# Kernel tuning notes

Measured on AMD Instinct MI355X. Metric: run time of the kernel, lower is better.

The kernel has to match this reference:

```python
import jax, jax.numpy as jnp
import numpy as np

T, B, H, L = 512, 32, 512, 2  # seq_len, batch, hidden_size, num_layers (input_size == H)


def _lstm_layer(x, Wih, Whh, bih, bhh):
    """x: [T,B,D]; Wih: [4H,D]; Whh: [4H,H]; biases: [4H]. Returns [T,B,H]."""
    # Precompute input contribution for all timesteps (one big GEMM).
    x_proj = jnp.einsum('tbd,gd->tbg', x, Wih) + bih + bhh  # [T,B,4H]
    h0 = jnp.zeros((x.shape[1], H), x.dtype)
    c0 = jnp.zeros((x.shape[1], H), x.dtype)

    def step(carry, xp):
        h, c = carry
        z = xp + h @ Whh.T  # [B,4H]
        i = jax.nn.sigmoid(z[:, 0 * H:1 * H])
        f = jax.nn.sigmoid(z[:, 1 * H:2 * H])
        g = jnp.tanh(z[:, 2 * H:3 * H])
        o = jax.nn.sigmoid(z[:, 3 * H:4 * H])
        c_new = f * c + i * g
        h_new = o * jnp.tanh(c_new)
        return (h_new, c_new), h_new

    (_, _), ys = jax.lax.scan(step, (h0, c0), x_proj)
    return ys  # [T,B,H]


def setup_inputs() -> dict:
    key = jax.random.key(0)
    k1, k2, k3, k4, k5 = jax.random.split(key, 5)
    scale = 1.0 / np.sqrt(H)  # torch Linear default init range ~ U(-1/sqrt(fan_in), ...)
    return {
        'seq_inputs': jax.random.normal(k1, (T, B, H), jnp.float32),
        'W_ih': jax.random.normal(k2, (L, 4 * H, H), jnp.float32) * scale,
        'W_hh': jax.random.normal(k3, (L, 4 * H, H), jnp.float32) * scale,
        'b_ih': jax.random.normal(k4, (L, 4 * H), jnp.float32) * scale,
        'b_hh': jax.random.normal(k5, (L, 4 * H), jnp.float32) * scale,
    }


def reference(seq_inputs, W_ih, W_hh, b_ih, b_hh):
    x = seq_inputs
    for l in range(L):  # small fixed layer loop
        x = _lstm_layer(x, W_ih[l], W_hh[l], b_ih[l], b_hh[l])
    return x  # [T,B,H] last-layer hidden sequence
```

## Files before the change

### kernel.cpp

```cpp
#include <hip/hip_runtime.h>


typedef _Float16 half8_t __attribute__((ext_vector_type(8)));
typedef _Float16 half4_t __attribute__((ext_vector_type(4)));
typedef float f32x4 __attribute__((ext_vector_type(4)));
typedef unsigned int u32;
typedef unsigned short u16;

#define T_LEN 512
#define BATCH 32
#define HID 512
#define SLOT 16384
#define LW (2048 * 512)

__device__ __forceinline__ float fast_sigmoid(float x) {
  return 1.f / (1.f + __expf(-x));
}
__device__ __forceinline__ float fast_tanh(float x) {
  return 1.f - 2.f / (1.f + __expf(2.f * x));
}
__device__ __forceinline__ u32 epoch_peek(const u32* p) {
  return __hip_atomic_load(p, __ATOMIC_RELAXED, __HIP_MEMORY_SCOPE_AGENT);
}

__global__ __launch_bounds__(256) void convert_k(
    const float4* __restrict__ x,
    const float4* __restrict__ wih,
    const float4* __restrict__ whh,
    const float* __restrict__ bih, const float* __restrict__ bhh,
    half4_t* __restrict__ xh, half4_t* __restrict__ wihh, half4_t* __restrict__ whhh,
    float* __restrict__ bsum) {
  const int N4X = 2097152, N4W = 524288, TOT = N4X + 2 * N4W;
  int gid = blockIdx.x * 256 + threadIdx.x;
  for (int i = gid; i < TOT; i += gridDim.x * 256) {
    float4 v;
    half4_t* dst;
    if (i < N4X) { v = x[i]; dst = xh + i; }
    else if (i < N4X + N4W) { v = wih[i - N4X]; dst = wihh + (i - N4X); }
    else { v = whh[i - N4X - N4W]; dst = whhh + (i - N4X - N4W); }
    half4_t h;
    h[0] = (_Float16)v.x; h[1] = (_Float16)v.y; h[2] = (_Float16)v.z; h[3] = (_Float16)v.w;
    *dst = h;
  }
  if (gid < 4096) bsum[gid] = bih[gid] + bhh[gid];
}

__global__ __launch_bounds__(128, 1) void lstm_fused(
    const _Float16* __restrict__ x0h,
    const _Float16* __restrict__ wih16,
    const _Float16* __restrict__ whh16,
    const float* __restrict__ bsum,
    _Float16* h0seq,
    _Float16* h1seq,
    u32* epoch0, u32* epoch1,
    float* outf) {
  int bid = blockIdx.x;
  int layer = bid >> 6, wg = bid & 63;
  int tid = threadIdx.x;
  int ln = tid & 63;
  int q = ln >> 4, l15 = ln & 15;
  int m0 = (tid >> 6) * 16;

  const _Float16* wih_l = wih16 + (size_t)layer * LW;
  const _Float16* whh_l = whh16 + (size_t)layer * LW;
  half8_t wx[2][16], wh[2][16];
  float bv[2];
#pragma unroll
  for (int j = 0; j < 2; ++j) {
    int nl = j * 16 + l15;
    int grow = (nl >> 3) * 512 + wg * 8 + (nl & 7);
    size_t ro = (size_t)grow * 512;
#pragma unroll
    for (int kc = 0; kc < 16; ++kc) {
      wx[j][kc] = *(const half8_t*)(wih_l + ro + kc * 32 + q * 8);
      wh[j][kc] = *(const half8_t*)(whh_l + ro + kc * 32 + q * 8);
    }
    bv[j] = bsum[layer * 2048 + grow];
  }

  const _Float16* xbase = layer ? (h0seq + SLOT) : x0h;
  _Float16* hself = layer ? h1seq : h0seq;
  u32* eself = layer ? epoch1 : epoch0;

  int cb = tid >> 2;
  int cp = tid & 3;
  int col0 = wg * 8 + cp * 2;
  float cst0 = 0.f, cst1 = 0.f;

  __shared__ float Zs[4 * 297];

  for (int t = 1; t <= T_LEN; ++t) {
    const _Float16* xsrc = xbase + (size_t)(t - 1) * SLOT;
    const _Float16* hsrc = hself + (size_t)(t - 1) * SLOT;
    f32x4 acc0 = {}, acc1 = {};
    half8_t af[16];

    if (layer == 0) {
#pragma unroll
      for (int kc = 0; kc < 16; ++kc)
        af[kc] = *(const half8_t*)(xsrc + (m0 + l15) * HID + kc * 32 + q * 8);
#pragma unroll
      for (int kc = 0; kc < 16; ++kc) {
        acc0 = __builtin_amdgcn_mfma_f32_16x16x32_f16(af[kc], wx[0][kc], acc0, 0, 0, 0);
        acc1 = __builtin_amdgcn_mfma_f32_16x16x32_f16(af[kc], wx[1][kc], acc1, 0, 0, 0);
      }
      u32 tgt = 64u * (u32)(t - 1);
      while (epoch_peek(epoch0) < tgt) { __builtin_amdgcn_s_sleep(1); }
      asm volatile("" ::: "memory");
    } else {
      u32 tgt0 = 64u * (u32)t, tgt1 = 64u * (u32)(t - 1);
      while (epoch_peek(epoch0) < tgt0 || epoch_peek(epoch1) < tgt1) {
        __builtin_amdgcn_s_sleep(1);
      }
      asm volatile("" ::: "memory");
#pragma unroll
      for (int kc = 0; kc < 16; ++kc)
        af[kc] = *(const half8_t*)(xsrc + (m0 + l15) * HID + kc * 32 + q * 8);
#pragma unroll
      for (int kc = 0; kc < 16; ++kc) {
        acc0 = __builtin_amdgcn_mfma_f32_16x16x32_f16(af[kc], wx[0][kc], acc0, 0, 0, 0);
        acc1 = __builtin_amdgcn_mfma_f32_16x16x32_f16(af[kc], wx[1][kc], acc1, 0, 0, 0);
      }
    }

#pragma unroll
    for (int kc = 0; kc < 16; ++kc)
      af[kc] = *(const half8_t*)(hsrc + (m0 + l15) * HID + kc * 32 + q * 8);
#pragma unroll
    for (int kc = 0; kc < 16; ++kc) {
      acc0 = __builtin_amdgcn_mfma_f32_16x16x32_f16(af[kc], wh[0][kc], acc0, 0, 0, 0);
      acc1 = __builtin_amdgcn_mfma_f32_16x16x32_f16(af[kc], wh[1][kc], acc1, 0, 0, 0);
    }

#pragma unroll
    for (int j = 0; j < 2; ++j) {
      int nl = j * 16 + l15, g = nl >> 3, c = nl & 7;
      const f32x4& a = j ? acc1 : acc0;
#pragma unroll
      for (int r = 0; r < 4; ++r)
        Zs[g * 297 + (m0 + q * 4 + r) * 9 + c] = a[r] + bv[j];
    }
    __syncthreads();

    float h0, h1;
    {
      float zi0 = Zs[0 * 297 + cb * 9 + cp * 2], zi1 = Zs[0 * 297 + cb * 9 + cp * 2 + 1];
      float zf0 = Zs[1 * 297 + cb * 9 + cp * 2], zf1 = Zs[1 * 297 + cb * 9 + cp * 2 + 1];
      float zg0 = Zs[2 * 297 + cb * 9 + cp * 2], zg1 = Zs[2 * 297 + cb * 9 + cp * 2 + 1];
      float zo0 = Zs[3 * 297 + cb * 9 + cp * 2], zo1 = Zs[3 * 297 + cb * 9 + cp * 2 + 1];
      float i0 = fast_sigmoid(zi0), f0 = fast_sigmoid(zf0), g0 = fast_tanh(zg0), o0 = fast_sigmoid(zo0);
      float i1 = fast_sigmoid(zi1), f1 = fast_sigmoid(zf1), g1 = fast_tanh(zg1), o1 = fast_sigmoid(zo1);
      cst0 = f0 * cst0 + i0 * g0;
      cst1 = f1 * cst1 + i1 * g1;
      h0 = o0 * fast_tanh(cst0);
      h1 = o1 * fast_tanh(cst1);
      u32 hp = (u32)__builtin_bit_cast(u16, (_Float16)h0) |
               ((u32)__builtin_bit_cast(u16, (_Float16)h1) << 16);
      u32* hdst = (u32*)(hself + (size_t)t * SLOT + cb * HID + col0);
      __hip_atomic_store(hdst, hp, __ATOMIC_RELAXED, __HIP_MEMORY_SCOPE_AGENT);
    }
    __syncthreads();
    if (tid == 0)
      (void)__hip_atomic_fetch_add(eself, 1u, __ATOMIC_RELAXED, __HIP_MEMORY_SCOPE_AGENT);
    if (layer) {
      float2 o2; o2.x = h0; o2.y = h1;
      *(float2*)(outf + (size_t)(t - 1) * SLOT + cb * HID + col0) = o2;
    }
  }
}

extern "C" void kernel_launch(void* const* d_in, const int* in_sizes, int n_in,
                              void* d_out, int out_size, void* d_ws, size_t ws_size,
                              hipStream_t stream) {
  const float* x = (const float*)d_in[0];
  const float* Wih = (const float*)d_in[1];
  const float* Whh = (const float*)d_in[2];
  const float* bih = (const float*)d_in[3];
  const float* bhh = (const float*)d_in[4];
  char* ws = (char*)d_ws;
  const size_t OFF_X0H = 0;
  const size_t OFF_H0SEQ = 16777216;
  const size_t OFF_H1SEQ = 33587200;
  const size_t OFF_WIH = 50397184;
  const size_t OFF_WHH = 54591488;
  const size_t OFF_BSUM = 58785792;
  const size_t OFF_EPOCH0 = 58802176;
  const size_t OFF_EPOCH1 = 58802432;
  const size_t TOTAL = 58802688;
  if (ws_size < TOTAL) return;
  _Float16* x0h = (_Float16*)(ws + OFF_X0H);
  _Float16* h0seq = (_Float16*)(ws + OFF_H0SEQ);
  _Float16* h1seq = (_Float16*)(ws + OFF_H1SEQ);
  _Float16* wihh = (_Float16*)(ws + OFF_WIH);
  _Float16* whhh = (_Float16*)(ws + OFF_WHH);
  float* bsum = (float*)(ws + OFF_BSUM);
  u32* epoch0 = (u32*)(ws + OFF_EPOCH0);
  u32* epoch1 = (u32*)(ws + OFF_EPOCH1);

  hipMemsetAsync(ws + OFF_EPOCH0, 0, 512, stream);
  hipMemsetAsync(ws + OFF_H0SEQ, 0, 32768, stream);
  hipMemsetAsync(ws + OFF_H1SEQ, 0, 32768, stream);
  convert_k<<<3072, 256, 0, stream>>>((const float4*)x, (const float4*)Wih,
                                      (const float4*)Whh, bih, bhh,
                                      (half4_t*)x0h, (half4_t*)wihh, (half4_t*)whhh, bsum);
  lstm_fused<<<128, 128, 0, stream>>>(x0h, wihh, whhh, bsum, h0seq, h1seq,
                                      epoch0, epoch1, (float*)d_out);
}
```

Before: 3.388 ms.

## Precompute layer-0 input projection with a tiled GEMM and relax per-step barriers

Layer 0's input contribution is now computed for all timesteps up front by a separate LDS-tiled MFMA GEMM (fp16 output with biases folded in), so the recurrent loop only does the Whh matmul for layer 0. Layer 0 prefetches its projected gates before spinning on the epoch counter. The Zs scratch is double-buffered by step parity, which lets the trailing __syncthreads be replaced by a vmcnt wait plus a per-wave epoch increment, with targets doubled to 128. The cost is an extra kernel, a 64MB fp16 intermediate, and fp16 rounding of the preactivations.

```diff
diff --git a/kernel.cpp b/kernel.cpp
--- a/kernel.cpp
+++ b/kernel.cpp
@@ -3,6 +3,7 @@
 
 typedef _Float16 half8_t __attribute__((ext_vector_type(8)));
 typedef _Float16 half4_t __attribute__((ext_vector_type(4)));
+typedef _Float16 half2_t __attribute__((ext_vector_type(2)));
 typedef float f32x4 __attribute__((ext_vector_type(4)));
 typedef unsigned int u32;
 typedef unsigned short u16;
@@ -22,80 +23,163 @@
 __device__ __forceinline__ u32 epoch_peek(const u32* p) {
   return __hip_atomic_load(p, __ATOMIC_RELAXED, __HIP_MEMORY_SCOPE_AGENT);
 }
-
-__global__ __launch_bounds__(256) void convert_k(
-    const float4* __restrict__ x,
-    const float4* __restrict__ wih,
-    const float4* __restrict__ whh,
-    const float* __restrict__ bih, const float* __restrict__ bhh,
-    half4_t* __restrict__ xh, half4_t* __restrict__ wihh, half4_t* __restrict__ whhh,
-    float* __restrict__ bsum) {
-  const int N4X = 2097152, N4W = 524288, TOT = N4X + 2 * N4W;
+__device__ __forceinline__ void async_copy16(const void* gsrc, void* ldst) {
+  __builtin_amdgcn_global_load_lds(
+      (const __attribute__((address_space(1))) u32*)gsrc,
+      (__attribute__((address_space(3))) u32*)ldst,
+      16, 0, 0);
+}
+
+__global__ __launch_bounds__(256) void convert_w(
+    const float4* __restrict__ wih, const float4* __restrict__ whh,
+    half4_t* __restrict__ wihh, half4_t* __restrict__ whhh) {
+  const int N4W = 524288;
   int gid = blockIdx.x * 256 + threadIdx.x;
-  for (int i = gid; i < TOT; i += gridDim.x * 256) {
+  for (int i = gid; i < 2 * N4W; i += gridDim.x * 256) {
     float4 v;
     half4_t* dst;
-    if (i < N4X) { v = x[i]; dst = xh + i; }
-    else if (i < N4X + N4W) { v = wih[i - N4X]; dst = wihh + (i - N4X); }
-    else { v = whh[i - N4X - N4W]; dst = whhh + (i - N4X - N4W); }
+    if (i < N4W) { v = wih[i]; dst = wihh + i; }
+    else { v = whh[i - N4W]; dst = whhh + (i - N4W); }
     half4_t h;
     h[0] = (_Float16)v.x; h[1] = (_Float16)v.y; h[2] = (_Float16)v.z; h[3] = (_Float16)v.w;
     *dst = h;
   }
-  if (gid < 4096) bsum[gid] = bih[gid] + bhh[gid];
+}
+
+__global__ __launch_bounds__(256) void gemm_xproj(
+    const float* __restrict__ A, const _Float16* __restrict__ W,
+    const float* __restrict__ bih, const float* __restrict__ bhh,
+    _Float16* __restrict__ C) {
+  __shared__ _Float16 As[128 * 64];
+  __shared__ _Float16 Bs[128 * 64];
+  int bx = blockIdx.x;
+  int tn = bx & 15, tm = bx >> 4;
+  int m0 = tm * 128, n0 = tn * 128;
+  int tid = threadIdx.x, wv = tid >> 6, ln = tid & 63;
+  int wm = wv & 1, wn = wv >> 1;
+  int q = ln >> 4, cc = ln & 15;
+  int am = tid >> 1, afq0 = (tid & 1) * 8;
+  f32x4 acc[4][4] = {};
+  for (int k0 = 0; k0 < 512; k0 += 64) {
+#pragma unroll
+    for (int i = 0; i < 8; ++i) {
+      int fq = afq0 + i;
+      float4 v = *(const float4*)(A + (size_t)(m0 + am) * 512 + k0 + fq * 4);
+      half4_t h;
+      h[0] = (_Float16)v.x; h[1] = (_Float16)v.y; h[2] = (_Float16)v.z; h[3] = (_Float16)v.w;
+      int c = fq >> 1, sub = fq & 1;
+      *(half4_t*)(As + am * 64 + (c ^ (am & 7)) * 8 + sub * 4) = h;
+    }
+#pragma unroll
+    for (int j = 0; j < 4; ++j) {
+      int p = (wv * 4 + j) * 64 + ln;
+      int m = p >> 3, pc = p & 7, kg = pc ^ (m & 7);
+      async_copy16(W + (size_t)(n0 + m) * 512 + k0 + kg * 8, (void*)(Bs + (p - ln) * 8));
+    }
+    __syncthreads();
+    for (int kc = 0; kc < 2; ++kc) {
+      half8_t af[4], bf[4];
+#pragma unroll
+      for (int i = 0; i < 4; ++i) {
+        int m = wm * 64 + i * 16 + cc;
+        int kg = (kc * 4 + q) ^ (m & 7);
+        af[i] = *(const half8_t*)(As + m * 64 + kg * 8);
+        int n = wn * 64 + i * 16 + cc;
+        int kg2 = (kc * 4 + q) ^ (n & 7);
+        bf[i] = *(const half8_t*)(Bs + n * 64 + kg2 * 8);
+      }
+#pragma unroll
+      for (int i = 0; i < 4; ++i)
+#pragma unroll
+        for (int j2 = 0; j2 < 4; ++j2)
+          acc[i][j2] = __builtin_amdgcn_mfma_f32_16x16x32_f16(af[i], bf[j2], acc[i][j2], 0, 0, 0);
+    }
+    __syncthreads();
+  }
+#pragma unroll
+  for (int j2 = 0; j2 < 4; ++j2) {
+    int n = n0 + wn * 64 + j2 * 16 + cc;
+    float bv = bih[n] + bhh[n];
+#pragma unroll
+    for (int i = 0; i < 4; ++i) {
+      int mbase = m0 + wm * 64 + i * 16 + q * 4;
+#pragma unroll
+      for (int r = 0; r < 4; ++r)
+        C[(size_t)(mbase + r) * 2048 + n] = (_Float16)(acc[i][j2][r] + bv);
+    }
+  }
 }
 
 __global__ __launch_bounds__(128, 1) void lstm_fused(
-    const _Float16* __restrict__ x0h,
+    const _Float16* __restrict__ xproj,
     const _Float16* __restrict__ wih16,
     const _Float16* __restrict__ whh16,
-    const float* __restrict__ bsum,
+    const float* __restrict__ bih, const float* __restrict__ bhh,
     _Float16* h0seq,
     _Float16* h1seq,
     u32* epoch0, u32* epoch1,
     float* outf) {
   int bid = blockIdx.x;
   int layer = bid >> 6, wg = bid & 63;
-  int tid = threadIdx.x;
-  int ln = tid & 63;
+  int tid = threadIdx.x, ln = tid & 63;
   int q = ln >> 4, l15 = ln & 15;
   int m0 = (tid >> 6) * 16;
-
-  const _Float16* wih_l = wih16 + (size_t)layer * LW;
+  int cb = tid >> 2, cp = tid & 3;
+  int col0 = wg * 8 + cp * 2;
+
   const _Float16* whh_l = whh16 + (size_t)layer * LW;
-  half8_t wx[2][16], wh[2][16];
-  float bv[2];
+  half8_t wh[2][16];
 #pragma unroll
   for (int j = 0; j < 2; ++j) {
     int nl = j * 16 + l15;
     int grow = (nl >> 3) * 512 + wg * 8 + (nl & 7);
     size_t ro = (size_t)grow * 512;
 #pragma unroll
-    for (int kc = 0; kc < 16; ++kc) {
-      wx[j][kc] = *(const half8_t*)(wih_l + ro + kc * 32 + q * 8);
+    for (int kc = 0; kc < 16; ++kc)
       wh[j][kc] = *(const half8_t*)(whh_l + ro + kc * 32 + q * 8);
-    }
-    bv[j] = bsum[layer * 2048 + grow];
-  }
-
-  const _Float16* xbase = layer ? (h0seq + SLOT) : x0h;
+  }
+  half8_t wx[2][16];
+  float bv[2] = {0.f, 0.f};
+  if (layer) {
+    const _Float16* wih_l = wih16 + (size_t)LW;
+#pragma unroll
+    for (int j = 0; j < 2; ++j) {
+      int nl = j * 16 + l15;
+      int grow = (nl >> 3) * 512 + wg * 8 + (nl & 7);
+      size_t ro = (size_t)grow * 512;
+#pragma unroll
+      for (int kc = 0; kc < 16; ++kc)
+        wx[j][kc] = *(const half8_t*)(wih_l + ro + kc * 32 + q * 8);
+      bv[j] = bih[2048 + grow] + bhh[2048 + grow];
+    }
+  }
+
   _Float16* hself = layer ? h1seq : h0seq;
   u32* eself = layer ? epoch1 : epoch0;
-
-  int cb = tid >> 2;
-  int cp = tid & 3;
-  int col0 = wg * 8 + cp * 2;
   float cst0 = 0.f, cst1 = 0.f;
 
-  __shared__ float Zs[4 * 297];
+  __shared__ float Zs[2][1188];
 
   for (int t = 1; t <= T_LEN; ++t) {
-    const _Float16* xsrc = xbase + (size_t)(t - 1) * SLOT;
-    const _Float16* hsrc = hself + (size_t)(t - 1) * SLOT;
+    int par = t & 1;
     f32x4 acc0 = {}, acc1 = {};
     half8_t af[16];
+    u32 zxw[4];
 
     if (layer == 0) {
+      const _Float16* zxp = xproj + (size_t)((t - 1) * 32 + cb) * 2048 + col0;
+#pragma unroll
+      for (int g = 0; g < 4; ++g) zxw[g] = *(const u32*)(zxp + g * 512);
+      u32 tgt = 128u * (u32)(t - 1);
+      while (epoch_peek(epoch0) < tgt) { __builtin_amdgcn_s_sleep(1); }
+      asm volatile("" ::: "memory");
+    } else {
+      u32 tgt0 = 128u * (u32)t, tgt1 = 128u * (u32)(t - 1);
+      while (epoch_peek(epoch0) < tgt0 || epoch_peek(epoch1) < tgt1) {
+        __builtin_amdgcn_s_sleep(1);
+      }
+      asm volatile("" ::: "memory");
+      const _Float16* xsrc = h0seq + (size_t)t * SLOT;
 #pragma unroll
       for (int kc = 0; kc < 16; ++kc)
         af[kc] = *(const half8_t*)(xsrc + (m0 + l15) * HID + kc * 32 + q * 8);
@@ -104,25 +188,9 @@
         acc0 = __builtin_amdgcn_mfma_f32_16x16x32_f16(af[kc], wx[0][kc], acc0, 0, 0, 0);
         acc1 = __builtin_amdgcn_mfma_f32_16x16x32_f16(af[kc], wx[1][kc], acc1, 0, 0, 0);
       }
-      u32 tgt = 64u * (u32)(t - 1);
-      while (epoch_peek(epoch0) < tgt) { __builtin_amdgcn_s_sleep(1); }
-      asm volatile("" ::: "memory");
-    } else {
-      u32 tgt0 = 64u * (u32)t, tgt1 = 64u * (u32)(t - 1);
-      while (epoch_peek(epoch0) < tgt0 || epoch_peek(epoch1) < tgt1) {
-        __builtin_amdgcn_s_sleep(1);
-      }
-      asm volatile("" ::: "memory");
-#pragma unroll
-      for (int kc = 0; kc < 16; ++kc)
-        af[kc] = *(const half8_t*)(xsrc + (m0 + l15) * HID + kc * 32 + q * 8);
-#pragma unroll
-      for (int kc = 0; kc < 16; ++kc) {
-        acc0 = __builtin_amdgcn_mfma_f32_16x16x32_f16(af[kc], wx[0][kc], acc0, 0, 0, 0);
-        acc1 = __builtin_amdgcn_mfma_f32_16x16x32_f16(af[kc], wx[1][kc], acc1, 0, 0, 0);
-      }
-    }
-
+    }
+
+    const _Float16* hsrc = hself + (size_t)(t - 1) * SLOT;
 #pragma unroll
     for (int kc = 0; kc < 16; ++kc)
       af[kc] = *(const half8_t*)(hsrc + (m0 + l15) * HID + kc * 32 + q * 8);
@@ -138,16 +206,26 @@
       const f32x4& a = j ? acc1 : acc0;
 #pragma unroll
       for (int r = 0; r < 4; ++r)
-        Zs[g * 297 + (m0 + q * 4 + r) * 9 + c] = a[r] + bv[j];
+        Zs[par][g * 297 + (m0 + q * 4 + r) * 9 + c] = a[r] + bv[j];
     }
     __syncthreads();
 
     float h0, h1;
     {
-      float zi0 = Zs[0 * 297 + cb * 9 + cp * 2], zi1 = Zs[0 * 297 + cb * 9 + cp * 2 + 1];
-      float zf0 = Zs[1 * 297 + cb * 9 + cp * 2], zf1 = Zs[1 * 297 + cb * 9 + cp * 2 + 1];
-      float zg0 = Zs[2 * 297 + cb * 9 + cp * 2], zg1 = Zs[2 * 297 + cb * 9 + cp * 2 + 1];
-      float zo0 = Zs[3 * 297 + cb * 9 + cp * 2], zo1 = Zs[3 * 297 + cb * 9 + cp * 2 + 1];
+      float zi0 = Zs[par][0 * 297 + cb * 9 + cp * 2], zi1 = Zs[par][0 * 297 + cb * 9 + cp * 2 + 1];
+      float zf0 = Zs[par][1 * 297 + cb * 9 + cp * 2], zf1 = Zs[par][1 * 297 + cb * 9 + cp * 2 + 1];
+      float zg0 = Zs[par][2 * 297 + cb * 9 + cp * 2], zg1 = Zs[par][2 * 297 + cb * 9 + cp * 2 + 1];
+      float zo0 = Zs[par][3 * 297 + cb * 9 + cp * 2], zo1 = Zs[par][3 * 297 + cb * 9 + cp * 2 + 1];
+      if (layer == 0) {
+        half2_t z0 = __builtin_bit_cast(half2_t, zxw[0]);
+        half2_t z1 = __builtin_bit_cast(half2_t, zxw[1]);
+        half2_t z2 = __builtin_bit_cast(half2_t, zxw[2]);
+        half2_t z3 = __builtin_bit_cast(half2_t, zxw[3]);
+        zi0 += (float)z0[0]; zi1 += (float)z0[1];
+        zf0 += (float)z1[0]; zf1 += (float)z1[1];
+        zg0 += (float)z2[0]; zg1 += (float)z2[1];
+        zo0 += (float)z3[0]; zo1 += (float)z3[1];
+      }
       float i0 = fast_sigmoid(zi0), f0 = fast_sigmoid(zf0), g0 = fast_tanh(zg0), o0 = fast_sigmoid(zo0);
       float i1 = fast_sigmoid(zi1), f1 = fast_sigmoid(zf1), g1 = fast_tanh(zg1), o1 = fast_sigmoid(zo1);
       cst0 = f0 * cst0 + i0 * g0;
@@ -159,8 +237,8 @@
       u32* hdst = (u32*)(hself + (size_t)t * SLOT + cb * HID + col0);
       __hip_atomic_store(hdst, hp, __ATOMIC_RELAXED, __HIP_MEMORY_SCOPE_AGENT);
     }
-    __syncthreads();
-    if (tid == 0)
+    asm volatile("s_waitcnt vmcnt(0)" ::: "memory");
+    if (ln == 0)
       (void)__hip_atomic_fetch_add(eself, 1u, __ATOMIC_RELAXED, __HIP_MEMORY_SCOPE_AGENT);
     if (layer) {
       float2 o2; o2.x = h0; o2.y = h1;
@@ -178,31 +256,28 @@
   const float* bih = (const float*)d_in[3];
   const float* bhh = (const float*)d_in[4];
   char* ws = (char*)d_ws;
-  const size_t OFF_X0H = 0;
-  const size_t OFF_H0SEQ = 16777216;
-  const size_t OFF_H1SEQ = 33587200;
-  const size_t OFF_WIH = 50397184;
-  const size_t OFF_WHH = 54591488;
-  const size_t OFF_BSUM = 58785792;
-  const size_t OFF_EPOCH0 = 58802176;
-  const size_t OFF_EPOCH1 = 58802432;
-  const size_t TOTAL = 58802688;
+  const size_t OFF_XPROJ = 0;
+  const size_t OFF_H0 = 67108864;
+  const size_t OFF_H1 = 83918848;
+  const size_t OFF_WIH = 100728832;
+  const size_t OFF_WHH = 104923136;
+  const size_t OFF_EPOCH = 109117440;
+  const size_t TOTAL = 109117952;
   if (ws_size < TOTAL) return;
-  _Float16* x0h = (_Float16*)(ws + OFF_X0H);
-  _Float16* h0seq = (_Float16*)(ws + OFF_H0SEQ);
-  _Float16* h1seq = (_Float16*)(ws + OFF_H1SEQ);
+  _Float16* xproj = (_Float16*)(ws + OFF_XPROJ);
+  _Float16* h0seq = (_Float16*)(ws + OFF_H0);
+  _Float16* h1seq = (_Float16*)(ws + OFF_H1);
   _Float16* wihh = (_Float16*)(ws + OFF_WIH);
   _Float16* whhh = (_Float16*)(ws + OFF_WHH);
-  float* bsum = (float*)(ws + OFF_BSUM);
-  u32* epoch0 = (u32*)(ws + OFF_EPOCH0);
-  u32* epoch1 = (u32*)(ws + OFF_EPOCH1);
-
-  hipMemsetAsync(ws + OFF_EPOCH0, 0, 512, stream);
-  hipMemsetAsync(ws + OFF_H0SEQ, 0, 32768, stream);
-  hipMemsetAsync(ws + OFF_H1SEQ, 0, 32768, stream);
-  convert_k<<<3072, 256, 0, stream>>>((const float4*)x, (const float4*)Wih,
-                                      (const float4*)Whh, bih, bhh,
-                                      (half4_t*)x0h, (half4_t*)wihh, (half4_t*)whhh, bsum);
-  lstm_fused<<<128, 128, 0, stream>>>(x0h, wihh, whhh, bsum, h0seq, h1seq,
-                                      epoch0, epoch1, (float*)d_out);
-}
+  u32* epoch0 = (u32*)(ws + OFF_EPOCH);
+  u32* epoch1 = (u32*)(ws + OFF_EPOCH + 256);
+
+  hipMemsetAsync(ws + OFF_EPOCH, 0, 512, stream);
+  hipMemsetAsync(ws + OFF_H0, 0, 32768, stream);
+  hipMemsetAsync(ws + OFF_H1, 0, 32768, stream);
+  convert_w<<<2048, 256, 0, stream>>>((const float4*)Wih, (const float4*)Whh,
+                                      (half4_t*)wihh, (half4_t*)whhh);
+  gemm_xproj<<<2048, 256, 0, stream>>>(x, wihh, bih, bhh, xproj);
+  lstm_fused<<<128, 128, 0, stream>>>(xproj, wihh, whhh, bih, bhh,
+                                      h0seq, h1seq, epoch0, epoch1, (float*)d_out);
+}
```

Measured after the change: 4.355 ms. 28.5% more time.
